# Kernel tuning notes

Hardware: AMD Instinct MI355X
Metric: run time of the kernel (lower is better)

Reference implementation:

```python
import jax, jax.numpy as jnp
import numpy as np

NUM_ITERS = 3  # num_iterations init arg


def squash(t, axis):
    # scale = ||t||^2 / (1+||t||^2); out = scale * t / ||t||
    sn = jnp.sum(t * t, axis=axis, keepdims=True)
    return (sn / (1.0 + sn)) * t / jnp.sqrt(sn)


def setup_inputs() -> dict:
    key = jax.random.key(0)
    k1, k2, k3 = jax.random.split(key, 3)
    B, I, O, DI, DO = 2048, 64, 32, 16, 16
    x = jax.random.normal(k1, (B, DI, I), dtype=jnp.float32)
    route_weights = jax.random.normal(k2, (O, I, DO, DI), dtype=jnp.float32)
    noise = 0.01 * jax.random.normal(k3, (O, I, DO, DI), dtype=jnp.float32)
    return {"x": x, "route_weights": route_weights, "noise": noise}


def reference(x, route_weights, noise):
    # random=True branch: perturbed routing weights
    W = route_weights + noise                      # [O,I,do,di]
    xt = jnp.transpose(x, (0, 2, 1))               # [B,I,di]
    # priors[b,o,i,d] = sum_e W[o,i,d,e] * xt[b,i,e]  (trailing singleton dim dropped)
    priors = jnp.einsum('oide,bie->boid', W, xt)   # [B,O,I,do]
    logits = jnp.zeros_like(priors)
    out = None
    for it in range(NUM_ITERS):
        probs = jax.nn.softmax(logits, axis=2)     # over input capsules I
        out = squash(jnp.sum(probs * priors, axis=2, keepdims=True), axis=3)  # [B,O,1,do]
        if it != NUM_ITERS - 1:
            logits = logits + priors * out         # routing-by-agreement update
    out = out[:, :, 0, :]                          # squeeze -> [B,O,do]
    # unsqueeze(0).transpose(2,1) -> [1,O,B,do]
    return jnp.transpose(out[None], (0, 2, 1, 3))
```

## Files before the change

### kernel.cpp

```cpp
#include <hip/hip_runtime.h>


#define THREADS 512

__global__ __launch_bounds__(THREADS) void routing_kernel(
    const float* __restrict__ x,
    const float* __restrict__ rw,
    const float* __restrict__ ns,
    float* __restrict__ out)
{
    extern __shared__ float lds[];
    float* xlds = lds + 8192;

    const int tid  = threadIdx.x;
    const int w    = tid >> 6;
    const int lane = tid & 63;

    const int o  = blockIdx.x >> 6;
    const int bc = blockIdx.x & 63;
    const int bbase = bc * 32;

    float wq0[16], wq1[16];
    {
        const int base = (o * 64 + lane) * 256 + w * 32;
        #pragma unroll
        for (int eq = 0; eq < 4; ++eq) {
            const float4 a0 = *reinterpret_cast<const float4*>(rw + base + eq * 4);
            const float4 n0 = *reinterpret_cast<const float4*>(ns + base + eq * 4);
            wq0[4*eq+0] = a0.x + n0.x;  wq0[4*eq+1] = a0.y + n0.y;
            wq0[4*eq+2] = a0.z + n0.z;  wq0[4*eq+3] = a0.w + n0.w;
            const float4 a1 = *reinterpret_cast<const float4*>(rw + base + 16 + eq * 4);
            const float4 n1 = *reinterpret_cast<const float4*>(ns + base + 16 + eq * 4);
            wq1[4*eq+0] = a1.x + n1.x;  wq1[4*eq+1] = a1.y + n1.y;
            wq1[4*eq+2] = a1.z + n1.z;  wq1[4*eq+3] = a1.w + n1.w;
        }
    }

    const int d0 = 2 * w, d1 = 2 * w + 1;
    float* pw0 = lds + d0 * 64 + ((((lane >> 2) ^ (d0 & 7)) << 2) | (lane & 3));
    float* pw1 = lds + d1 * 64 + ((((lane >> 2) ^ (d1 & 7)) << 2) | (lane & 3));

    const int qB  = lane >> 4;
    const int dB  = lane & 15;
    const int swz = dB & 7;
    const float4* prbase = reinterpret_cast<const float4*>(lds) + (w * 16 + dB) * 16;
    const float4* pr0 = prbase + ((4 * qB + 0) ^ swz);
    const float4* pr1 = prbase + ((4 * qB + 1) ^ swz);
    const float4* pr2 = prbase + ((4 * qB + 2) ^ swz);
    const float4* pr3 = prbase + ((4 * qB + 3) ^ swz);

    const float* xrb = xlds + lane * 16 + ((lane >> 3) << 2);

    const int il = lane & 15, ih = lane >> 4;
    float* xwb = xlds + w * 1056 + il * 64 + ((il >> 1) << 2) + ih;
    float* xw0 = xwb + 0;
    float* xw1 = xwb + 4;
    float* xw2 = xwb + 8;
    float* xw3 = xwb + 12;

    const float4* xsrc0 = reinterpret_cast<const float4*>(x) + bbase * 256
                        + (w * 256 + lane);

    const int outbase = (o * 2048 + bbase + w) * 16 + dB;

    float4 xb0 = xsrc0[0];
    float4 xb1 = xsrc0[64];
    float4 xb2 = xsrc0[128];
    float4 xb3 = xsrc0[192];
    xw0[0] = xb0.x;  xw0[16] = xb0.y;  xw0[32] = xb0.z;  xw0[48] = xb0.w;
    xw1[0] = xb1.x;  xw1[16] = xb1.y;  xw1[32] = xb1.z;  xw1[48] = xb1.w;
    xw2[0] = xb2.x;  xw2[16] = xb2.y;  xw2[32] = xb2.z;  xw2[48] = xb2.w;
    xw3[0] = xb3.x;  xw3[16] = xb3.y;  xw3[32] = xb3.z;  xw3[48] = xb3.w;
    __syncthreads();

    #pragma unroll
    for (int s = 0; s < 4; ++s) {
        #pragma unroll
        for (int bb = 0; bb < 8; ++bb) {
            const float4 v0 = *reinterpret_cast<const float4*>(xrb + bb * 1056 + 0);
            const float4 v1 = *reinterpret_cast<const float4*>(xrb + bb * 1056 + 4);
            const float4 v2 = *reinterpret_cast<const float4*>(xrb + bb * 1056 + 8);
            const float4 v3 = *reinterpret_cast<const float4*>(xrb + bb * 1056 + 12);
            float a0 = 0.f, a1 = 0.f;
            a0 = fmaf(wq0[0],  v0.x, a0);  a1 = fmaf(wq1[0],  v0.x, a1);
            a0 = fmaf(wq0[1],  v0.y, a0);  a1 = fmaf(wq1[1],  v0.y, a1);
            a0 = fmaf(wq0[2],  v0.z, a0);  a1 = fmaf(wq1[2],  v0.z, a1);
            a0 = fmaf(wq0[3],  v0.w, a0);  a1 = fmaf(wq1[3],  v0.w, a1);
            a0 = fmaf(wq0[4],  v1.x, a0);  a1 = fmaf(wq1[4],  v1.x, a1);
            a0 = fmaf(wq0[5],  v1.y, a0);  a1 = fmaf(wq1[5],  v1.y, a1);
            a0 = fmaf(wq0[6],  v1.z, a0);  a1 = fmaf(wq1[6],  v1.z, a1);
            a0 = fmaf(wq0[7],  v1.w, a0);  a1 = fmaf(wq1[7],  v1.w, a1);
            a0 = fmaf(wq0[8],  v2.x, a0);  a1 = fmaf(wq1[8],  v2.x, a1);
            a0 = fmaf(wq0[9],  v2.y, a0);  a1 = fmaf(wq1[9],  v2.y, a1);
            a0 = fmaf(wq0[10], v2.z, a0);  a1 = fmaf(wq1[10], v2.z, a1);
            a0 = fmaf(wq0[11], v2.w, a0);  a1 = fmaf(wq1[11], v2.w, a1);
            a0 = fmaf(wq0[12], v3.x, a0);  a1 = fmaf(wq1[12], v3.x, a1);
            a0 = fmaf(wq0[13], v3.y, a0);  a1 = fmaf(wq1[13], v3.y, a1);
            a0 = fmaf(wq0[14], v3.z, a0);  a1 = fmaf(wq1[14], v3.z, a1);
            a0 = fmaf(wq0[15], v3.w, a0);  a1 = fmaf(wq1[15], v3.w, a1);
            pw0[bb * 1024] = a0;
            pw1[bb * 1024] = a1;
        }
        __syncthreads();

        float p[16];
        {
            const float4 v0 = *pr0, v1 = *pr1, v2 = *pr2, v3 = *pr3;
            p[0]=v0.x; p[1]=v0.y; p[2]=v0.z; p[3]=v0.w;
            p[4]=v1.x; p[5]=v1.y; p[6]=v1.z; p[7]=v1.w;
            p[8]=v2.x; p[9]=v2.y; p[10]=v2.z; p[11]=v2.w;
            p[12]=v3.x; p[13]=v3.y; p[14]=v3.z; p[15]=v3.w;
        }

        if (s < 3) {
            const float4* xsrc = xsrc0 + (s + 1) * 2048;
            xb0 = xsrc[0];  xb1 = xsrc[64];  xb2 = xsrc[128];  xb3 = xsrc[192];
        }

        float t0 = (p[0]+p[1]) + (p[2]+p[3]);
        float t1 = (p[4]+p[5]) + (p[6]+p[7]);
        float t2 = (p[8]+p[9]) + (p[10]+p[11]);
        float t3 = (p[12]+p[13]) + (p[14]+p[15]);
        float part = (t0 + t1) + (t2 + t3);
        part += __shfl_xor(part, 16);
        part += __shfl_xor(part, 32);
        float sv = part * (1.0f / 64.0f);

        float sn = sv * sv;
        sn += __shfl_xor(sn, 1); sn += __shfl_xor(sn, 2);
        sn += __shfl_xor(sn, 4); sn += __shfl_xor(sn, 8);
        float factor = __builtin_amdgcn_sqrtf(sn)
                     * __builtin_amdgcn_rcpf(1.0f + sn);
        float Vsum = sv * factor;

        #pragma unroll
        for (int it = 0; it < 2; ++it) {
            const float c = Vsum * 1.44269504089f;
            float e0, e1, e2, e3;
            float dd0, dd1, dd2, dd3, nn0, nn1, nn2, nn3;
            e0 = __builtin_amdgcn_exp2f(p[0] * c);
            e1 = __builtin_amdgcn_exp2f(p[1] * c);
            e2 = __builtin_amdgcn_exp2f(p[2] * c);
            e3 = __builtin_amdgcn_exp2f(p[3] * c);
            dd0 = e0; dd1 = e1; dd2 = e2; dd3 = e3;
            nn0 = e0 * p[0]; nn1 = e1 * p[1]; nn2 = e2 * p[2]; nn3 = e3 * p[3];
            e0 = __builtin_amdgcn_exp2f(p[4] * c);
            e1 = __builtin_amdgcn_exp2f(p[5] * c);
            e2 = __builtin_amdgcn_exp2f(p[6] * c);
            e3 = __builtin_amdgcn_exp2f(p[7] * c);
            dd0 += e0; dd1 += e1; dd2 += e2; dd3 += e3;
            nn0 = fmaf(e0, p[4], nn0); nn1 = fmaf(e1, p[5], nn1);
            nn2 = fmaf(e2, p[6], nn2); nn3 = fmaf(e3, p[7], nn3);
            e0 = __builtin_amdgcn_exp2f(p[8] * c);
            e1 = __builtin_amdgcn_exp2f(p[9] * c);
            e2 = __builtin_amdgcn_exp2f(p[10] * c);
            e3 = __builtin_amdgcn_exp2f(p[11] * c);
            dd0 += e0; dd1 += e1; dd2 += e2; dd3 += e3;
            nn0 = fmaf(e0, p[8], nn0);  nn1 = fmaf(e1, p[9], nn1);
            nn2 = fmaf(e2, p[10], nn2); nn3 = fmaf(e3, p[11], nn3);
            e0 = __builtin_amdgcn_exp2f(p[12] * c);
            e1 = __builtin_amdgcn_exp2f(p[13] * c);
            e2 = __builtin_amdgcn_exp2f(p[14] * c);
            e3 = __builtin_amdgcn_exp2f(p[15] * c);
            dd0 += e0; dd1 += e1; dd2 += e2; dd3 += e3;
            nn0 = fmaf(e0, p[12], nn0); nn1 = fmaf(e1, p[13], nn1);
            nn2 = fmaf(e2, p[14], nn2); nn3 = fmaf(e3, p[15], nn3);

            float den = (dd0 + dd1) + (dd2 + dd3);
            float num = (nn0 + nn1) + (nn2 + nn3);
            den += __shfl_xor(den, 16); den += __shfl_xor(den, 32);
            num += __shfl_xor(num, 16); num += __shfl_xor(num, 32);
            sv = num * __builtin_amdgcn_rcpf(den);
            sn = sv * sv;
            sn += __shfl_xor(sn, 1); sn += __shfl_xor(sn, 2);
            sn += __shfl_xor(sn, 4); sn += __shfl_xor(sn, 8);
            factor = __builtin_amdgcn_sqrtf(sn)
                   * __builtin_amdgcn_rcpf(1.0f + sn);
            Vsum += sv * factor;
        }

        if (qB == 0)
            out[outbase + s * 128] = sv * factor;

        if (s < 3) {
            xw0[0] = xb0.x;  xw0[16] = xb0.y;  xw0[32] = xb0.z;  xw0[48] = xb0.w;
            xw1[0] = xb1.x;  xw1[16] = xb1.y;  xw1[32] = xb1.z;  xw1[48] = xb1.w;
            xw2[0] = xb2.x;  xw2[16] = xb2.y;  xw2[32] = xb2.z;  xw2[48] = xb2.w;
            xw3[0] = xb3.x;  xw3[16] = xb3.y;  xw3[32] = xb3.z;  xw3[48] = xb3.w;
        }
        __syncthreads();
    }
}

extern "C" void kernel_launch(void* const* d_in, const int* in_sizes, int n_in,
                              void* d_out, int out_size, void* d_ws, size_t ws_size,
                              hipStream_t stream) {
    const float* x  = (const float*)d_in[0];
    const float* rw = (const float*)d_in[1];
    const float* ns = (const float*)d_in[2];
    float* out = (float*)d_out;
    (void)d_ws; (void)ws_size; (void)in_sizes; (void)n_in; (void)out_size;

    const int grid = 32 * 64;
    routing_kernel<<<grid, THREADS, 66560, stream>>>(x, rw, ns, out);
}
```

Before: 83.08 us.

## Double batch per block and precompute summed weights in workspace kernel

Each block now handles 64 batch rows in 8 stages instead of 32 rows in 4, which halves the grid and so halves how often each block's register-resident weight slice is loaded. When workspace is large enough, a separate small kernel adds route_weights and noise once into the workspace, and the routing kernel reads only the summed weights. This cuts redundant global weight traffic and adds at the cost of an extra launch and fewer blocks (1024), which may reduce occupancy and load balance across CUs.

After: 76.59 us. 1.08x faster.

```diff
diff --git a/kernel.cpp b/kernel.cpp
--- a/kernel.cpp
+++ b/kernel.cpp
@@ -3,6 +3,19 @@
 
 #define THREADS 512
 
+__global__ __launch_bounds__(256) void wsum_kernel(
+    const float* __restrict__ rw, const float* __restrict__ ns,
+    float* __restrict__ w2)
+{
+    const int i = blockIdx.x * 256 + threadIdx.x;
+    const float4 a = reinterpret_cast<const float4*>(rw)[i];
+    const float4 n = reinterpret_cast<const float4*>(ns)[i];
+    float4 r;
+    r.x = a.x + n.x;  r.y = a.y + n.y;  r.z = a.z + n.z;  r.w = a.w + n.w;
+    reinterpret_cast<float4*>(w2)[i] = r;
+}
+
+template <bool PRE>
 __global__ __launch_bounds__(THREADS) void routing_kernel(
     const float* __restrict__ x,
     const float* __restrict__ rw,
@@ -16,23 +29,32 @@
     const int w    = tid >> 6;
     const int lane = tid & 63;
 
-    const int o  = blockIdx.x >> 6;
-    const int bc = blockIdx.x & 63;
-    const int bbase = bc * 32;
+    const int o  = blockIdx.x >> 5;
+    const int bc = blockIdx.x & 31;
+    const int bbase = bc * 64;
 
     float wq0[16], wq1[16];
     {
         const int base = (o * 64 + lane) * 256 + w * 32;
         #pragma unroll
         for (int eq = 0; eq < 4; ++eq) {
-            const float4 a0 = *reinterpret_cast<const float4*>(rw + base + eq * 4);
-            const float4 n0 = *reinterpret_cast<const float4*>(ns + base + eq * 4);
-            wq0[4*eq+0] = a0.x + n0.x;  wq0[4*eq+1] = a0.y + n0.y;
-            wq0[4*eq+2] = a0.z + n0.z;  wq0[4*eq+3] = a0.w + n0.w;
-            const float4 a1 = *reinterpret_cast<const float4*>(rw + base + 16 + eq * 4);
-            const float4 n1 = *reinterpret_cast<const float4*>(ns + base + 16 + eq * 4);
-            wq1[4*eq+0] = a1.x + n1.x;  wq1[4*eq+1] = a1.y + n1.y;
-            wq1[4*eq+2] = a1.z + n1.z;  wq1[4*eq+3] = a1.w + n1.w;
+            if (PRE) {
+                const float4 a0 = *reinterpret_cast<const float4*>(rw + base + eq * 4);
+                wq0[4*eq+0] = a0.x;  wq0[4*eq+1] = a0.y;
+                wq0[4*eq+2] = a0.z;  wq0[4*eq+3] = a0.w;
+                const float4 a1 = *reinterpret_cast<const float4*>(rw + base + 16 + eq * 4);
+                wq1[4*eq+0] = a1.x;  wq1[4*eq+1] = a1.y;
+                wq1[4*eq+2] = a1.z;  wq1[4*eq+3] = a1.w;
+            } else {
+                const float4 a0 = *reinterpret_cast<const float4*>(rw + base + eq * 4);
+                const float4 n0 = *reinterpret_cast<const float4*>(ns + base + eq * 4);
+                wq0[4*eq+0] = a0.x + n0.x;  wq0[4*eq+1] = a0.y + n0.y;
+                wq0[4*eq+2] = a0.z + n0.z;  wq0[4*eq+3] = a0.w + n0.w;
+                const float4 a1 = *reinterpret_cast<const float4*>(rw + base + 16 + eq * 4);
+                const float4 n1 = *reinterpret_cast<const float4*>(ns + base + 16 + eq * 4);
+                wq1[4*eq+0] = a1.x + n1.x;  wq1[4*eq+1] = a1.y + n1.y;
+                wq1[4*eq+2] = a1.z + n1.z;  wq1[4*eq+3] = a1.w + n1.w;
+            }
         }
     }
 
@@ -74,7 +96,7 @@
     __syncthreads();
 
     #pragma unroll
-    for (int s = 0; s < 4; ++s) {
+    for (int s = 0; s < 8; ++s) {
         #pragma unroll
         for (int bb = 0; bb < 8; ++bb) {
             const float4 v0 = *reinterpret_cast<const float4*>(xrb + bb * 1056 + 0);
@@ -112,7 +134,7 @@
             p[12]=v3.x; p[13]=v3.y; p[14]=v3.z; p[15]=v3.w;
         }
 
-        if (s < 3) {
+        if (s < 7) {
             const float4* xsrc = xsrc0 + (s + 1) * 2048;
             xb0 = xsrc[0];  xb1 = xsrc[64];  xb2 = xsrc[128];  xb3 = xsrc[192];
         }
@@ -182,7 +204,7 @@
         if (qB == 0)
             out[outbase + s * 128] = sv * factor;
 
-        if (s < 3) {
+        if (s < 7) {
             xw0[0] = xb0.x;  xw0[16] = xb0.y;  xw0[32] = xb0.z;  xw0[48] = xb0.w;
             xw1[0] = xb1.x;  xw1[16] = xb1.y;  xw1[32] = xb1.z;  xw1[48] = xb1.w;
             xw2[0] = xb2.x;  xw2[16] = xb2.y;  xw2[32] = xb2.z;  xw2[48] = xb2.w;
@@ -199,8 +221,16 @@
     const float* rw = (const float*)d_in[1];
     const float* ns = (const float*)d_in[2];
     float* out = (float*)d_out;
-    (void)d_ws; (void)ws_size; (void)in_sizes; (void)n_in; (void)out_size;
-
-    const int grid = 32 * 64;
-    routing_kernel<<<grid, THREADS, 66560, stream>>>(x, rw, ns, out);
+    (void)in_sizes; (void)n_in; (void)out_size;
+
+    const int grid = 32 * 32;
+    const size_t w2_bytes = 32u * 64u * 16u * 16u * sizeof(float);
+
+    if (ws_size >= w2_bytes) {
+        float* w2 = (float*)d_ws;
+        wsum_kernel<<<512, 256, 0, stream>>>(rw, ns, w2);
+        routing_kernel<true><<<grid, THREADS, 66560, stream>>>(x, w2, ns, out);
+    } else {
+        routing_kernel<false><<<grid, THREADS, 66560, stream>>>(x, rw, ns, out);
+    }
 }
```
